# Optimization experiments

Measured on AMD Instinct MI355X. Metric: run time of the kernel, lower is better.

Reference implementation:

```python
import jax, jax.numpy as jnp
import numpy as np

# ---- model constants (from init_kwargs) ----
HIDDEN = 4096
NUM_HEADS = 32
HEAD_DIM = HIDDEN // NUM_HEADS  # 128
ROPE_THETA = 10000.0
P8 = 512
P6 = 1024
P4 = HIDDEN - P8 - P6  # 2560
BLOCK = 32  # scale-factor block size (SFB* are sized out*p//32)


def _block_quant(x, bits):
    """Symmetric per-32-element-block fake quantization along the last dim.
    Emulates the dequantized math of the packed 4/6/8-bit tiers in mixedgemm."""
    qmax = 2.0 ** (bits - 1) - 1.0
    shp = x.shape
    xb = x.reshape(shp[:-1] + (shp[-1] // BLOCK, BLOCK))
    scale = jnp.maximum(jnp.max(jnp.abs(xb), axis=-1, keepdims=True) / qmax, 1e-8)
    dq = (jnp.clip(jnp.round(xb / scale), -qmax, qmax) * scale).reshape(shp)
    return dq


def _mixed_quant(x):
    """Split reordered features into [p4 | p6 | p8] tiers and quantize each."""
    xn, xs, xo = jnp.split(x, [P4, P4 + P6], axis=-1)
    return jnp.concatenate([_block_quant(xn, 4), _block_quant(xs, 6), _block_quant(xo, 8)], axis=-1)


def _qlinear(x, W, reorder_index):
    """reorder_quantize_x + mixedgemm.matmul (dequantized reference math).
    x: [T, in], W: [out, in] (stored already in reordered column order)."""
    xq = _mixed_quant(x[..., reorder_index])
    Wq = _mixed_quant(W)
    return xq @ Wq.T


def _rotate_half(x):
    h = x.shape[-1] // 2
    return jnp.concatenate([-x[..., h:], x[..., :h]], axis=-1)


def setup_inputs() -> dict:
    key = jax.random.key(0)
    k1, k2, k3, k4, k5 = jax.random.split(key, 5)
    B, S = 2, 2048
    hidden_states = jax.random.normal(k1, (B, S, HIDDEN), dtype=jnp.float32)
    Wq = jax.random.normal(k2, (HIDDEN, HIDDEN), dtype=jnp.float32) * 0.02
    Wk = jax.random.normal(k3, (HIDDEN, HIDDEN), dtype=jnp.float32) * 0.02
    Wv = jax.random.normal(k4, (HIDDEN, HIDDEN), dtype=jnp.float32) * 0.02
    Wo = jax.random.normal(k5, (HIDDEN, HIDDEN), dtype=jnp.float32) * 0.02
    position_ids = jnp.broadcast_to(jnp.arange(S, dtype=jnp.int32)[None, :], (B, S))
    reorder_index = jnp.arange(HIDDEN, dtype=jnp.int32)  # default identity reorder
    return {"hidden_states": hidden_states, "Wq": Wq, "Wk": Wk, "Wv": Wv,
            "Wo": Wo, "position_ids": position_ids, "reorder_index": reorder_index}


def reference(hidden_states, Wq, Wk, Wv, Wo, position_ids, reorder_index):
    B, S, H = hidden_states.shape
    x2 = hidden_states.reshape(B * S, H)

    q = _qlinear(x2, Wq, reorder_index).reshape(B, S, NUM_HEADS, HEAD_DIM)
    k = _qlinear(x2, Wk, reorder_index).reshape(B, S, NUM_HEADS, HEAD_DIM)
    v = _qlinear(x2, Wv, reorder_index).reshape(B, S, NUM_HEADS, HEAD_DIM)

    # LlamaRotaryEmbedding: cos/sin [B, S, head_dim], unsqueeze_dim=2 (broadcast over heads)
    inv_freq = 1.0 / (ROPE_THETA ** (jnp.arange(0, HEAD_DIM, 2, dtype=jnp.float32) / HEAD_DIM))
    freqs = position_ids.astype(jnp.float32)[..., None] * inv_freq  # [B, S, hd/2]
    emb = jnp.concatenate([freqs, freqs], axis=-1)                  # [B, S, hd]
    cos = jnp.cos(emb)[:, :, None, :]
    sin = jnp.sin(emb)[:, :, None, :]
    q = q * cos + _rotate_half(q) * sin
    k = k * cos + _rotate_half(k) * sin

    # causal SDPA over [B, nH, S, hd]
    qh = q.transpose(0, 2, 1, 3)
    kh = k.transpose(0, 2, 1, 3)
    vh = v.transpose(0, 2, 1, 3)
    scaling = 1.0 / jnp.sqrt(jnp.float32(HEAD_DIM))
    scores = jnp.einsum('bhqd,bhkd->bhqk', qh, kh) * scaling
    causal = jnp.tril(jnp.ones((S, S), dtype=bool))
    scores = jnp.where(causal[None, None], scores, jnp.finfo(scores.dtype).min)
    probs = jax.nn.softmax(scores, axis=-1)
    attn = jnp.einsum('bhqk,bhkd->bhqd', probs, vh)  # [B, nH, S, hd]

    attn = attn.transpose(0, 2, 1, 3).reshape(B * S, H)
    out = _qlinear(attn, Wo, reorder_index).reshape(B, S, H)
    return out
```

## Files before the change

kernel.cpp:

```cpp
#include <hip/hip_runtime.h>


typedef __bf16 bf16_t;
typedef __bf16 bf16x4 __attribute__((ext_vector_type(4)));
typedef __bf16 bf16x8 __attribute__((ext_vector_type(8)));
typedef float f32x4 __attribute__((ext_vector_type(4)));

#define MFMA16(a, b, c) __builtin_amdgcn_mfma_f32_16x16x32_bf16(a, b, c, 0, 0, 0)

__device__ __forceinline__ void split_bf16(float x, bf16_t& h, bf16_t& l) {
    h = (bf16_t)x;
    l = (bf16_t)(x - (float)h);
}

typedef const __attribute__((address_space(1))) void glb_v;
typedef __attribute__((address_space(3))) void lds_v;

__device__ __forceinline__ void gl_lds16(const void* g, void* l) {
    __builtin_amdgcn_global_load_lds((glb_v*)g, (lds_v*)l, 16, 0, 0);
}
__device__ __forceinline__ void gl_lds4(const void* g, void* l) {
    __builtin_amdgcn_global_load_lds((glb_v*)g, (lds_v*)l, 4, 0, 0);
}

template<int OUT_I8>
__global__ void quant_is(const float* __restrict__ srcf,
                         const bf16_t* __restrict__ shi, const bf16_t* __restrict__ slo,
                         const int* __restrict__ rid, int src_split, int gather,
                         signed char* __restrict__ qi8, bf16_t* __restrict__ qbf,
                         float* __restrict__ qsT) {
    long idx = ((long)blockIdx.x * 256 + threadIdx.x) << 2;
    int col = (int)(idx & 4095);
    long rowoff = idx & ~4095L;
    float v[4];
    float a = 0.f;
#pragma unroll
    for (int j = 0; j < 4; ++j) {
        int g = gather ? rid[col + j] : col + j;
        float x = src_split ? ((float)shi[rowoff + g] + (float)slo[rowoff + g])
                            : srcf[rowoff + g];
        v[j] = x;
        a = fmaxf(a, fabsf(x));
    }
#pragma unroll
    for (int off = 1; off < 8; off <<= 1) a = fmaxf(a, __shfl_xor(a, off, 64));
    float qmax = (col < 2560) ? 7.0f : (col < 3584 ? 31.0f : 127.0f);
    float scale = fmaxf(a / qmax, 1e-8f);
    float inv = 1.0f / scale;
    if (OUT_I8) {
        int pk = 0;
#pragma unroll
        for (int j = 0; j < 4; ++j) {
            float q = fminf(fmaxf(rintf(v[j] * inv), -qmax), qmax);
            pk |= (int)(unsigned char)(signed char)(int)q << (8 * j);
        }
        *(int*)&qi8[idx] = pk;
    } else {
        bf16x4 pk;
#pragma unroll
        for (int j = 0; j < 4; ++j) {
            float q = fminf(fmaxf(rintf(v[j] * inv), -qmax), qmax);
            pk[j] = (bf16_t)q;
        }
        *(bf16x4*)&qbf[idx] = pk;
    }
    if ((col & 31) == 0) qsT[((long)(col >> 5) << 12) + (idx >> 12)] = scale;
}

template<int OSPL>
__global__ __launch_bounds__(256, 2) void gemm_is(
    const signed char* __restrict__ Ai, const float* __restrict__ AsT,
    const bf16_t* __restrict__ Bi, const float* __restrict__ BsT,
    bf16_t* __restrict__ OHi, bf16_t* __restrict__ OLo, float* __restrict__ Of) {
    constexpr int K = 4096, N = 4096;
    __shared__ __align__(16) bf16_t sA[2][128 * 32];
    __shared__ __align__(16) bf16_t sB[2][128 * 32];
    __shared__ __align__(16) float  sS[2][256];

    const int tid = threadIdx.x;
    const int bid = blockIdx.x;
    const int xcd = bid & 7, j = bid >> 3;
    const int bx = xcd * 4 + (j & 3), by = j >> 2;
    const int rowBase = by << 7, colBase = bx << 7;
    const int lane = tid & 63, wave = tid >> 6;
    const int wr = (wave >> 1) << 6, wc = (wave & 1) << 6;
    const int n16 = lane & 15, quad = lane >> 4;

    const int arow = tid >> 1, achk = (tid & 1) << 4;
    const long aSrc = (long)(rowBase + arow) * K + achk;
    const int aDst = arow * 64 + achk * 2;
    const int brow = tid >> 2, bchk = (tid & 3) << 3;
    const long bSrc0 = (long)(colBase + brow) * K + bchk;
    const long bSrc1 = (long)(colBase + 64 + brow) * K + bchk;
    const int bDst = tid << 4;
    const int sIsB = wave >> 1;
    const float* sPtr = (sIsB ? BsT + colBase : AsT + rowBase) + ((wave & 1) << 6) + lane;
    const int sDst = (sIsB ? 512 : 0) + ((wave & 1) << 8) + (lane << 2);

    f32x4 acc[4][4];
#pragma unroll
    for (int m = 0; m < 4; ++m)
#pragma unroll
        for (int n = 0; n < 4; ++n) acc[m][n] = (f32x4){0.f, 0.f, 0.f, 0.f};

    int4 aReg;

#define ISSUE(BUF, KB) do {                                                   \
    char* _b = (char*)sB[BUF]; char* _s = (char*)sS[BUF];                     \
    const int _k0 = (KB) << 5;                                                \
    gl_lds16(Bi + bSrc0 + _k0, _b + bDst);                                    \
    gl_lds16(Bi + bSrc1 + _k0, _b + 4096 + bDst);                             \
    gl_lds4(sPtr + ((long)(KB) << 12), _s + sDst);                            \
    aReg = *(const int4*)(Ai + aSrc + _k0);                                   \
} while (0)

#define FINISH(BUF) do {                                                      \
    asm volatile("s_waitcnt vmcnt(0)" ::: "memory");                          \
    const signed char* _pc = (const signed char*)&aReg;                       \
    bf16x8 _v0, _v1;                                                          \
    _Pragma("unroll")                                                         \
    for (int _j = 0; _j < 8; ++_j) {                                          \
        _v0[_j] = (bf16_t)(float)_pc[_j];                                     \
        _v1[_j] = (bf16_t)(float)_pc[8 + _j];                                 \
    }                                                                         \
    *(bf16x8*)((char*)sA[BUF] + aDst) = _v0;                                  \
    *(bf16x8*)((char*)sA[BUF] + aDst + 16) = _v1;                             \
    asm volatile("s_waitcnt lgkmcnt(0)" ::: "memory");                        \
    __builtin_amdgcn_s_barrier();                                             \
    asm volatile("" ::: "memory");                                            \
} while (0)

    ISSUE(0, 0);
    FINISH(0);

    for (int kb = 0; kb < 128; ++kb) {
        const int cur = kb & 1;
        if (kb < 127) ISSUE(cur ^ 1, kb + 1);

        const char* pA = (const char*)sA[cur];
        const char* pB = (const char*)sB[cur];
        const char* pS = (const char*)sS[cur];
        bf16x8 a[4], b[4];
        f32x4 asv[4];
        float bsv[4];
#pragma unroll
        for (int m = 0; m < 4; ++m) {
            a[m] = *(const bf16x8*)(pA + (wr + (m << 4) + n16) * 64 + (quad << 4));
            asv[m] = *(const f32x4*)(pS + ((wr + (m << 4) + (quad << 2)) << 2));
        }
#pragma unroll
        for (int n = 0; n < 4; ++n) {
            b[n] = *(const bf16x8*)(pB + (wc + (n << 4) + n16) * 64 + (quad << 4));
            bsv[n] = *(const float*)(pS + 512 + ((wc + (n << 4) + n16) << 2));
        }
        const f32x4 z = (f32x4){0.f, 0.f, 0.f, 0.f};
#pragma unroll
        for (int m = 0; m < 4; ++m)
#pragma unroll
            for (int n = 0; n < 4; ++n) {
                f32x4 sc = MFMA16(a[m], b[n], z);
                float bn = bsv[n];
#pragma unroll
                for (int r = 0; r < 4; ++r)
                    acc[m][n][r] = fmaf(asv[m][r] * bn, sc[r], acc[m][n][r]);
            }

        if (kb < 127) FINISH(cur ^ 1);
    }
#undef ISSUE
#undef FINISH

#pragma unroll
    for (int m = 0; m < 4; ++m)
#pragma unroll
        for (int n = 0; n < 4; ++n) {
            int row = rowBase + wr + (m << 4) + (quad << 2);
            int col = colBase + wc + (n << 4) + n16;
#pragma unroll
            for (int r = 0; r < 4; ++r) {
                if (OSPL) {
                    bf16_t h, l;
                    split_bf16(acc[m][n][r], h, l);
                    OHi[(long)(row + r) * N + col] = h;
                    OLo[(long)(row + r) * N + col] = l;
                } else {
                    Of[(long)(row + r) * N + col] = acc[m][n][r];
                }
            }
        }
}

__global__ void rope2(bf16_t* __restrict__ qh, bf16_t* __restrict__ ql,
                      bf16_t* __restrict__ kh, bf16_t* __restrict__ kl,
                      const int* __restrict__ pos) {
    int t = blockIdx.x;
    int tid = threadIdx.x;
    __shared__ float cs[64], sn[64];
    if (tid < 64) {
        float invf = (float)pow(10000.0, -(double)tid / 64.0);
        float ang = (float)pos[t] * invf;
        cs[tid] = (float)cos((double)ang);
        sn[tid] = (float)sin((double)ang);
    }
    __syncthreads();
#pragma unroll
    for (int i = 0; i < 8; ++i) {
        int l = i * 256 + tid;
        int hh = l >> 6, d = l & 63;
        long base = (long)t * 4096 + hh * 128 + d;
        float c = cs[d], s = sn[d];
        float a0 = (float)qh[base] + (float)ql[base];
        float a1 = (float)qh[base + 64] + (float)ql[base + 64];
        float r0 = a0 * c - a1 * s, r1 = a1 * c + a0 * s;
        bf16_t x, y;
        split_bf16(r0, x, y); qh[base] = x;      ql[base] = y;
        split_bf16(r1, x, y); qh[base + 64] = x; ql[base + 64] = y;
        float b0 = (float)kh[base] + (float)kl[base];
        float b1 = (float)kh[base + 64] + (float)kl[base + 64];
        r0 = b0 * c - b1 * s; r1 = b1 * c + b0 * s;
        split_bf16(r0, x, y); kh[base] = x;      kl[base] = y;
        split_bf16(r1, x, y); kh[base + 64] = x; kl[base + 64] = y;
    }
}

__global__ void transpose_vt(const ushort* __restrict__ vh, const ushort* __restrict__ vl,
                             ushort* __restrict__ th, ushort* __restrict__ tl) {
    __shared__ ushort t0[64][68];
    __shared__ ushort t1[64][68];
    int ct = blockIdx.x, tt = blockIdx.y, tid = threadIdx.x;
#pragma unroll
    for (int i = 0; i < 16; ++i) {
        int l = i * 256 + tid, r = l >> 6, c = l & 63;
        long idx = (long)(tt * 64 + r) * 4096 + ct * 64 + c;
        t0[r][c] = vh[idx];
        t1[r][c] = vl[idx];
    }
    __syncthreads();
#pragma unroll
    for (int i = 0; i < 16; ++i) {
        int l = i * 256 + tid, dr = l >> 6, sc = l & 63;
        int colg = ct * 64 + dr, hh = colg >> 7, dl = colg & 127;
        int tok = tt * 64 + sc, b = tok >> 11, s = tok & 2047;
        long o = (long)((b * 32 + hh) * 128 + dl) * 2048 + s;
        th[o] = t0[sc][dr];
        tl[o] = t1[sc][dr];
    }
}

__global__ __launch_bounds__(256, 2) void flash_attn3(
    const bf16_t* __restrict__ qhp, const bf16_t* __restrict__ qlp,
    const bf16_t* __restrict__ khp, const bf16_t* __restrict__ klp,
    const bf16_t* __restrict__ vth, const bf16_t* __restrict__ vtl,
    bf16_t* __restrict__ ohi, bf16_t* __restrict__ olo) {
    __shared__ __align__(16) char smem[75776];

    const int bid = blockIdx.x;
    const int xcd = bid & 7, ixd = bid >> 3;
    const int bh = (xcd << 3) + (ixd >> 4);
    const int qt = 15 - (ixd & 15);
    const int b = bh >> 5, h = bh & 31;
    const int tid = threadIdx.x;
    const int wave = tid >> 6, lane = tid & 63;
    const int n16 = lane & 15, quad = lane >> 4;
    const long tokB = (long)b * 2048;
    const int q0 = qt * 128 + wave * 32;
    const float scale = 0.08838834764831845f;

    bf16_t (*pH)[40] = (bf16_t (*)[40])(smem + 65536 + wave * 2560);
    bf16_t (*pL)[40] = (bf16_t (*)[40])(smem + 65536 + wave * 2560 + 1280);

    bf16x8 qhF[2][4], qlF[2][4];
#pragma unroll
    for (int m = 0; m < 2; ++m) {
        long qoff = (tokB + q0 + m * 16 + n16) * 4096 + h * 128 + quad * 8;
#pragma unroll
        for (int f = 0; f < 4; ++f) {
            qhF[m][f] = *(const bf16x8*)&qhp[qoff + f * 32];
            qlF[m][f] = *(const bf16x8*)&qlp[qoff + f * 32];
        }
    }

    const int kr0 = wave * 8 + quad;
    const int kc0 = ((((lane & 15) << 4) ^ (quad << 4)) >> 1);
    const int kc1 = ((((lane & 15) << 4) ^ ((4 + quad) << 4)) >> 1);
    const int kd0 = kr0 * 256 + ((lane & 15) << 4);
    const int vr0 = wave * 32 + (lane >> 2);
    const int vc0 = ((((lane & 3) << 4) ^ (((lane >> 2) & 3) << 4)) >> 1);
    const int vd0 = vr0 * 64 + ((lane & 3) << 4);
    const long vrow_g = (long)(bh * 128 + vr0) * 2048;

#define STAGE(BUF, KB) do {                                                   \
    char* _bb = smem + ((BUF) << 15);                                         \
    const long _kt = tokB + (long)(KB) * 32;                                  \
    const long _g0 = (_kt + kr0) * 4096 + h * 128;                            \
    gl_lds16(khp + _g0 + kc0,           _bb + kd0);                           \
    gl_lds16(klp + _g0 + kc0,           _bb + 8192 + kd0);                    \
    gl_lds16(khp + _g0 + 4 * 4096 + kc1, _bb + 1024 + kd0);                   \
    gl_lds16(klp + _g0 + 4 * 4096 + kc1, _bb + 8192 + 1024 + kd0);            \
    const long _v0 = vrow_g + (KB) * 32 + vc0;                                \
    gl_lds16(vth + _v0,                 _bb + 16384 + vd0);                   \
    gl_lds16(vtl + _v0,                 _bb + 24576 + vd0);                   \
    gl_lds16(vth + _v0 + 16 * 2048,     _bb + 16384 + 1024 + vd0);            \
    gl_lds16(vtl + _v0 + 16 * 2048,     _bb + 24576 + 1024 + vd0);            \
} while (0)

    f32x4 o[2][8];
#pragma unroll
    for (int m = 0; m < 2; ++m)
#pragma unroll
        for (int dc = 0; dc < 8; ++dc) o[m][dc] = (f32x4){0.f, 0.f, 0.f, 0.f};
    float m_i[2][4], l_i[2][4];
#pragma unroll
    for (int m = 0; m < 2; ++m)
#pragma unroll
        for (int r = 0; r < 4; ++r) { m_i[m][r] = -1e30f; l_i[m][r] = 0.f; }

    const int nkb = 4 * qt + 4;
    const int lastkb = 4 * qt + wave;

    STAGE(0, 0);
    asm volatile("s_waitcnt vmcnt(0)" ::: "memory");
    __builtin_amdgcn_s_barrier();
    asm volatile("" ::: "memory");

    for (int kb = 0; kb < nkb; ++kb) {
        if (kb + 1 < nkb) STAGE((kb + 1) & 1, kb + 1);

        if (kb <= lastkb) {
            const char* bK = smem + ((kb & 1) << 15);
            const char* bV = bK + 16384;

            f32x4 s[2][2];
            const int rswz = (n16 & 7) << 4;
#pragma unroll
            for (int nt = 0; nt < 2; ++nt) {
                const int krow = nt * 16 + n16;
                bf16x8 kh[4], kl[4];
#pragma unroll
                for (int f = 0; f < 4; ++f) {
                    const int cb = ((f << 6) | (quad << 4)) ^ rswz;
                    kh[f] = *(const bf16x8*)(bK + krow * 256 + cb);
                    kl[f] = *(const bf16x8*)(bK + 8192 + krow * 256 + cb);
                }
#pragma unroll
                for (int m = 0; m < 2; ++m) {
                    f32x4 sc = (f32x4){0.f, 0.f, 0.f, 0.f};
#pragma unroll
                    for (int f = 0; f < 4; ++f) {
                        sc = MFMA16(qhF[m][f], kh[f], sc);
                        sc = MFMA16(qhF[m][f], kl[f], sc);
                        sc = MFMA16(qlF[m][f], kh[f], sc);
                    }
                    s[m][nt] = sc;
                }
            }

            if (kb == lastkb) {
                const int key0 = kb * 32 + n16;
#pragma unroll
                for (int m = 0; m < 2; ++m)
#pragma unroll
                    for (int nt = 0; nt < 2; ++nt)
#pragma unroll
                        for (int r = 0; r < 4; ++r) {
                            int qrow = q0 + m * 16 + quad * 4 + r;
                            s[m][nt][r] = (key0 + nt * 16 <= qrow) ? s[m][nt][r] * scale
                                                                   : -1e30f;
                        }
            } else {
#pragma unroll
                for (int m = 0; m < 2; ++m)
#pragma unroll
                    for (int nt = 0; nt < 2; ++nt)
#pragma unroll
                        for (int r = 0; r < 4; ++r) s[m][nt][r] *= scale;
            }

            float alpha[2][4];
#pragma unroll
            for (int m = 0; m < 2; ++m)
#pragma unroll
                for (int r = 0; r < 4; ++r) {
                    float mx = fmaxf(s[m][0][r], s[m][1][r]);
#pragma unroll
                    for (int off = 1; off < 16; off <<= 1) mx = fmaxf(mx, __shfl_xor(mx, off, 64));
                    float mnew = fmaxf(m_i[m][r], mx);
                    alpha[m][r] = expf(m_i[m][r] - mnew);
                    m_i[m][r] = mnew;
                    float p0 = expf(s[m][0][r] - mnew);
                    float p1 = expf(s[m][1][r] - mnew);
                    s[m][0][r] = p0;
                    s[m][1][r] = p1;
                    float sum = p0 + p1;
#pragma unroll
                    for (int off = 1; off < 16; off <<= 1) sum += __shfl_xor(sum, off, 64);
                    l_i[m][r] = l_i[m][r] * alpha[m][r] + sum;
                }

            bf16x8 ph2[2], pl2[2];
#pragma unroll
            for (int m = 0; m < 2; ++m) {
#pragma unroll
                for (int nt = 0; nt < 2; ++nt)
#pragma unroll
                    for (int r = 0; r < 4; ++r) {
                        bf16_t hh2, ll2;
                        split_bf16(s[m][nt][r], hh2, ll2);
                        pH[quad * 4 + r][nt * 16 + n16] = hh2;
                        pL[quad * 4 + r][nt * 16 + n16] = ll2;
                    }
                ph2[m] = *(const bf16x8*)&pH[n16][quad * 8];
                pl2[m] = *(const bf16x8*)&pL[n16][quad * 8];
            }

#pragma unroll
            for (int dc = 0; dc < 8; ++dc) {
                const int vrow = dc * 16 + n16;
                const int vcb = ((quad ^ (n16 & 3)) << 4);
                bf16x8 vh = *(const bf16x8*)(bV + vrow * 64 + vcb);
                bf16x8 vl = *(const bf16x8*)(bV + 8192 + vrow * 64 + vcb);
#pragma unroll
                for (int m = 0; m < 2; ++m) {
#pragma unroll
                    for (int r = 0; r < 4; ++r) o[m][dc][r] *= alpha[m][r];
                    o[m][dc] = MFMA16(ph2[m], vh, o[m][dc]);
                    o[m][dc] = MFMA16(ph2[m], vl, o[m][dc]);
                    o[m][dc] = MFMA16(pl2[m], vh, o[m][dc]);
                }
            }
        }

        asm volatile("s_waitcnt vmcnt(0)" ::: "memory");
        __builtin_amdgcn_s_barrier();
        asm volatile("" ::: "memory");
    }
#undef STAGE

#pragma unroll
    for (int m = 0; m < 2; ++m)
#pragma unroll
        for (int r = 0; r < 4; ++r) {
            float invl = 1.0f / l_i[m][r];
            long row = tokB + q0 + m * 16 + quad * 4 + r;
#pragma unroll
            for (int dc = 0; dc < 8; ++dc) {
                bf16_t hh2, ll2;
                split_bf16(o[m][dc][r] * invl, hh2, ll2);
                ohi[row * 4096 + h * 128 + dc * 16 + n16] = hh2;
                olo[row * 4096 + h * 128 + dc * 16 + n16] = ll2;
            }
        }
}

extern "C" void kernel_launch(void* const* d_in, const int* in_sizes, int n_in,
                              void* d_out, int out_size, void* d_ws, size_t ws_size,
                              hipStream_t stream) {
    const float* x  = (const float*)d_in[0];
    const float* Wq = (const float*)d_in[1];
    const float* Wk = (const float*)d_in[2];
    const float* Wv = (const float*)d_in[3];
    const float* Wo = (const float*)d_in[4];
    const int* pos  = (const int*)d_in[5];
    const int* rid  = (const int*)d_in[6];

    const size_t MB = 1024ull * 1024ull;
    char* ws = (char*)d_ws;
    bf16_t* QH = (bf16_t*)(ws);
    bf16_t* QL = (bf16_t*)(ws + 32 * MB);
    bf16_t* KH = (bf16_t*)(ws + 64 * MB);
    bf16_t* KL = (bf16_t*)(ws + 96 * MB);
    signed char* Xi = (signed char*)(ws + 128 * MB);
    float*  XsT = (float*)(ws + 144 * MB);
    float*  WsT = (float*)(ws + 146 * MB);
    bf16_t* Wi  = (bf16_t*)(ws + 160 * MB);
    bf16_t* VTh = (bf16_t*)(ws + 128 * MB);
    bf16_t* VTl = (bf16_t*)(ws + 160 * MB);
    signed char* Xi2 = (signed char*)(ws + 64 * MB);
    float*  Xs2T = (float*)(ws + 96 * MB);
    bf16_t* Wo_i = (bf16_t*)(ws + 128 * MB);
    float*  WoST = (float*)(ws + 160 * MB);
    bf16_t* OUh = (bf16_t*)d_out;
    bf16_t* OUl = (bf16_t*)((char*)d_out + 32 * MB);

    const int QG = 16384;

    quant_is<1><<<QG, 256, 0, stream>>>(x, nullptr, nullptr, rid, 0, 1, Xi, nullptr, XsT);

    quant_is<0><<<QG, 256, 0, stream>>>(Wq, nullptr, nullptr, rid, 0, 0, nullptr, Wi, WsT);
    gemm_is<1><<<1024, 256, 0, stream>>>(Xi, XsT, Wi, WsT, QH, QL, nullptr);
    quant_is<0><<<QG, 256, 0, stream>>>(Wk, nullptr, nullptr, rid, 0, 0, nullptr, Wi, WsT);
    gemm_is<1><<<1024, 256, 0, stream>>>(Xi, XsT, Wi, WsT, KH, KL, nullptr);
    quant_is<0><<<QG, 256, 0, stream>>>(Wv, nullptr, nullptr, rid, 0, 0, nullptr, Wi, WsT);
    gemm_is<1><<<1024, 256, 0, stream>>>(Xi, XsT, Wi, WsT, OUh, OUl, nullptr);

    rope2<<<4096, 256, 0, stream>>>(QH, QL, KH, KL, pos);

    transpose_vt<<<dim3(64, 64), 256, 0, stream>>>((const ushort*)OUh, (const ushort*)OUl,
                                                   (ushort*)VTh, (ushort*)VTl);

    flash_attn3<<<1024, 256, 0, stream>>>(QH, QL, KH, KL, VTh, VTl, OUh, OUl);

    quant_is<1><<<QG, 256, 0, stream>>>(nullptr, OUh, OUl, rid, 1, 1, Xi2, nullptr, Xs2T);
    quant_is<0><<<QG, 256, 0, stream>>>(Wo, nullptr, nullptr, rid, 0, 0, nullptr, Wo_i, WoST);
    gemm_is<0><<<1024, 256, 0, stream>>>(Xi2, Xs2T, Wo_i, WoST, nullptr, nullptr, (float*)d_out);

    (void)in_sizes; (void)n_in; (void)out_size; (void)ws_size;
}
```

Measured before the change: 2.381 ms.

## Triple-buffer and swizzle GEMM, vectorize quant/rope/transpose, add MFMA priority hints

New measurement: 2.186 ms. -8.2%, faster.

```diff
diff --git a/kernel.cpp b/kernel.cpp
--- a/kernel.cpp
+++ b/kernel.cpp
@@ -23,10 +23,10 @@
     __builtin_amdgcn_global_load_lds((glb_v*)g, (lds_v*)l, 4, 0, 0);
 }
 
-template<int OUT_I8>
+template<int OUT_I8, int SPLIT, int GATHER>
 __global__ void quant_is(const float* __restrict__ srcf,
                          const bf16_t* __restrict__ shi, const bf16_t* __restrict__ slo,
-                         const int* __restrict__ rid, int src_split, int gather,
+                         const int* __restrict__ rid,
                          signed char* __restrict__ qi8, bf16_t* __restrict__ qbf,
                          float* __restrict__ qsT) {
     long idx = ((long)blockIdx.x * 256 + threadIdx.x) << 2;
@@ -34,13 +34,20 @@
     long rowoff = idx & ~4095L;
     float v[4];
     float a = 0.f;
-#pragma unroll
-    for (int j = 0; j < 4; ++j) {
-        int g = gather ? rid[col + j] : col + j;
-        float x = src_split ? ((float)shi[rowoff + g] + (float)slo[rowoff + g])
+    if (!GATHER && !SPLIT) {
+        float4 f = *(const float4*)&srcf[idx];
+        v[0] = f.x; v[1] = f.y; v[2] = f.z; v[3] = f.w;
+#pragma unroll
+        for (int j = 0; j < 4; ++j) a = fmaxf(a, fabsf(v[j]));
+    } else {
+#pragma unroll
+        for (int j = 0; j < 4; ++j) {
+            int g = GATHER ? rid[col + j] : col + j;
+            float x = SPLIT ? ((float)shi[rowoff + g] + (float)slo[rowoff + g])
                             : srcf[rowoff + g];
-        v[j] = x;
-        a = fmaxf(a, fabsf(x));
+            v[j] = x;
+            a = fmaxf(a, fabsf(x));
+        }
     }
 #pragma unroll
     for (int off = 1; off < 8; off <<= 1) a = fmaxf(a, __shfl_xor(a, off, 64));
@@ -73,25 +80,29 @@
     const bf16_t* __restrict__ Bi, const float* __restrict__ BsT,
     bf16_t* __restrict__ OHi, bf16_t* __restrict__ OLo, float* __restrict__ Of) {
     constexpr int K = 4096, N = 4096;
-    __shared__ __align__(16) bf16_t sA[2][128 * 32];
-    __shared__ __align__(16) bf16_t sB[2][128 * 32];
-    __shared__ __align__(16) float  sS[2][256];
+    __shared__ __align__(16) bf16_t sA[3][128 * 32];
+    __shared__ __align__(16) bf16_t sB[3][128 * 32];
+    __shared__ __align__(16) float  sS[3][256];
 
     const int tid = threadIdx.x;
     const int bid = blockIdx.x;
-    const int xcd = bid & 7, j = bid >> 3;
-    const int bx = xcd * 4 + (j & 3), by = j >> 2;
+    const int xcd = bid & 7, jj = bid >> 3;
+    const int bx = xcd * 4 + (jj & 3), by = jj >> 2;
     const int rowBase = by << 7, colBase = bx << 7;
     const int lane = tid & 63, wave = tid >> 6;
     const int wr = (wave >> 1) << 6, wc = (wave & 1) << 6;
     const int n16 = lane & 15, quad = lane >> 4;
 
-    const int arow = tid >> 1, achk = (tid & 1) << 4;
-    const long aSrc = (long)(rowBase + arow) * K + achk;
-    const int aDst = arow * 64 + achk * 2;
-    const int brow = tid >> 2, bchk = (tid & 3) << 3;
-    const long bSrc0 = (long)(colBase + brow) * K + bchk;
-    const long bSrc1 = (long)(colBase + 64 + brow) * K + bchk;
+    const int arow = tid >> 1, acb = (tid & 1) << 4;
+    const long aSrc = (long)(rowBase + arow) * K + acb;
+    const int aswz = (arow & 3) << 4;
+    const int ac0 = (acb >> 3) << 4;
+    const int aDst0 = arow * 64 + (ac0 ^ aswz);
+    const int aDst1 = arow * 64 + ((ac0 + 16) ^ aswz);
+    const int brow = tid >> 2;
+    const int bcs = (((tid & 3) ^ (brow & 3)) << 3);
+    const long bSrc0 = (long)(colBase + brow) * K + bcs;
+    const long bSrc1 = (long)(colBase + 64 + brow) * K + bcs;
     const int bDst = tid << 4;
     const int sIsB = wave >> 1;
     const float* sPtr = (sIsB ? BsT + colBase : AsT + rowBase) + ((wave & 1) << 6) + lane;
@@ -103,72 +114,104 @@
 #pragma unroll
         for (int n = 0; n < 4; ++n) acc[m][n] = (f32x4){0.f, 0.f, 0.f, 0.f};
 
-    int4 aReg;
-
-#define ISSUE(BUF, KB) do {                                                   \
-    char* _b = (char*)sB[BUF]; char* _s = (char*)sS[BUF];                     \
-    const int _k0 = (KB) << 5;                                                \
+    int4 aRegA, aRegB;
+
+#define ISSUE(BUFI, KB, AR) do {                                              \
+    char* _b = (char*)sB[BUFI];                                               \
+    char* _s = (char*)sS[BUFI];                                               \
+    const long _k0 = (long)(KB) << 5;                                         \
     gl_lds16(Bi + bSrc0 + _k0, _b + bDst);                                    \
     gl_lds16(Bi + bSrc1 + _k0, _b + 4096 + bDst);                             \
     gl_lds4(sPtr + ((long)(KB) << 12), _s + sDst);                            \
-    aReg = *(const int4*)(Ai + aSrc + _k0);                                   \
+    AR = *(const int4*)(Ai + aSrc + _k0);                                     \
 } while (0)
 
-#define FINISH(BUF) do {                                                      \
-    asm volatile("s_waitcnt vmcnt(0)" ::: "memory");                          \
-    const signed char* _pc = (const signed char*)&aReg;                       \
+#define CVTW(BUFI, AR) do {                                                   \
+    const signed char* _pc = (const signed char*)&AR;                         \
     bf16x8 _v0, _v1;                                                          \
     _Pragma("unroll")                                                         \
-    for (int _j = 0; _j < 8; ++_j) {                                          \
-        _v0[_j] = (bf16_t)(float)_pc[_j];                                     \
-        _v1[_j] = (bf16_t)(float)_pc[8 + _j];                                 \
+    for (int _j2 = 0; _j2 < 8; ++_j2) {                                       \
+        _v0[_j2] = (bf16_t)(float)_pc[_j2];                                   \
+        _v1[_j2] = (bf16_t)(float)_pc[8 + _j2];                               \
     }                                                                         \
-    *(bf16x8*)((char*)sA[BUF] + aDst) = _v0;                                  \
-    *(bf16x8*)((char*)sA[BUF] + aDst + 16) = _v1;                             \
-    asm volatile("s_waitcnt lgkmcnt(0)" ::: "memory");                        \
-    __builtin_amdgcn_s_barrier();                                             \
-    asm volatile("" ::: "memory");                                            \
+    *(bf16x8*)((char*)sA[BUFI] + aDst0) = _v0;                                \
+    *(bf16x8*)((char*)sA[BUFI] + aDst1) = _v1;                                \
 } while (0)
 
-    ISSUE(0, 0);
-    FINISH(0);
-
-    for (int kb = 0; kb < 128; ++kb) {
-        const int cur = kb & 1;
-        if (kb < 127) ISSUE(cur ^ 1, kb + 1);
-
-        const char* pA = (const char*)sA[cur];
-        const char* pB = (const char*)sB[cur];
-        const char* pS = (const char*)sS[cur];
-        bf16x8 a[4], b[4];
-        f32x4 asv[4];
-        float bsv[4];
-#pragma unroll
-        for (int m = 0; m < 4; ++m) {
-            a[m] = *(const bf16x8*)(pA + (wr + (m << 4) + n16) * 64 + (quad << 4));
-            asv[m] = *(const f32x4*)(pS + ((wr + (m << 4) + (quad << 2)) << 2));
-        }
-#pragma unroll
-        for (int n = 0; n < 4; ++n) {
-            b[n] = *(const bf16x8*)(pB + (wc + (n << 4) + n16) * 64 + (quad << 4));
-            bsv[n] = *(const float*)(pS + 512 + ((wc + (n << 4) + n16) << 2));
-        }
-        const f32x4 z = (f32x4){0.f, 0.f, 0.f, 0.f};
-#pragma unroll
-        for (int m = 0; m < 4; ++m)
-#pragma unroll
-            for (int n = 0; n < 4; ++n) {
-                f32x4 sc = MFMA16(a[m], b[n], z);
-                float bn = bsv[n];
-#pragma unroll
-                for (int r = 0; r < 4; ++r)
-                    acc[m][n][r] = fmaf(asv[m][r] * bn, sc[r], acc[m][n][r]);
-            }
-
-        if (kb < 127) FINISH(cur ^ 1);
+#define WAITV(NN) asm volatile("s_waitcnt vmcnt(" #NN ")" ::: "memory")
+#define BARR() do { asm volatile("s_waitcnt lgkmcnt(0)" ::: "memory");        \
+    __builtin_amdgcn_s_barrier(); asm volatile("" ::: "memory"); } while (0)
+
+#define COMPUTE(BUFI) do {                                                    \
+    const char* _pA = (const char*)sA[BUFI];                                  \
+    const char* _pB = (const char*)sB[BUFI];                                  \
+    const float* _pS = sS[BUFI];                                              \
+    const int _rsw = (n16 & 3) << 4;                                          \
+    bf16x8 _a[4], _bv[4];                                                     \
+    f32x4 _as[4];                                                             \
+    float _bs[4];                                                             \
+    _Pragma("unroll")                                                         \
+    for (int _m = 0; _m < 4; ++_m) {                                          \
+        _a[_m] = *(const bf16x8*)(_pA + (wr + (_m << 4) + n16) * 64           \
+                                  + ((quad << 4) ^ _rsw));                    \
+        _as[_m] = *(const f32x4*)(_pS + wr + (_m << 4) + (quad << 2));        \
+    }                                                                         \
+    _Pragma("unroll")                                                         \
+    for (int _n = 0; _n < 4; ++_n) {                                          \
+        _bv[_n] = *(const bf16x8*)(_pB + (wc + (_n << 4) + n16) * 64          \
+                                   + ((quad << 4) ^ _rsw));                   \
+        _bs[_n] = _pS[128 + wc + (_n << 4) + n16];                            \
+    }                                                                         \
+    const f32x4 _z = (f32x4){0.f, 0.f, 0.f, 0.f};                             \
+    _Pragma("unroll")                                                         \
+    for (int _m = 0; _m < 4; ++_m)                                            \
+        _Pragma("unroll")                                                     \
+        for (int _n = 0; _n < 4; ++_n) {                                      \
+            f32x4 _sc = MFMA16(_a[_m], _bv[_n], _z);                          \
+            float _bn = _bs[_n];                                              \
+            _Pragma("unroll")                                                 \
+            for (int _r = 0; _r < 4; ++_r)                                    \
+                acc[_m][_n][_r] = fmaf(_as[_m][_r] * _bn, _sc[_r],            \
+                                       acc[_m][_n][_r]);                      \
+        }                                                                     \
+} while (0)
+
+    ISSUE(0, 0, aRegA);
+    ISSUE(1, 1, aRegB);
+    WAITV(4);
+    CVTW(0, aRegA);
+    BARR();
+
+    int bc = 0;
+    for (int kb = 0; kb < 128; kb += 2) {
+        int b1 = bc + 1; if (b1 >= 3) b1 -= 3;
+        int b2 = bc + 2; if (b2 >= 3) b2 -= 3;
+        if (kb + 2 < 128) {
+            ISSUE(b2, kb + 2, aRegA);
+            COMPUTE(bc);
+            WAITV(4);
+        } else {
+            COMPUTE(bc);
+            WAITV(0);
+        }
+        CVTW(b1, aRegB);
+        BARR();
+        if (kb + 3 < 128) {
+            ISSUE(bc, kb + 3, aRegB);
+            COMPUTE(b1);
+            WAITV(4);
+            CVTW(b2, aRegA);
+            BARR();
+        } else {
+            COMPUTE(b1);
+        }
+        bc = b2;
     }
 #undef ISSUE
-#undef FINISH
+#undef CVTW
+#undef WAITV
+#undef BARR
+#undef COMPUTE
 
 #pragma unroll
     for (int m = 0; m < 4; ++m)
@@ -203,47 +246,66 @@
         sn[tid] = (float)sin((double)ang);
     }
     __syncthreads();
-#pragma unroll
-    for (int i = 0; i < 8; ++i) {
-        int l = i * 256 + tid;
-        int hh = l >> 6, d = l & 63;
-        long base = (long)t * 4096 + hh * 128 + d;
-        float c = cs[d], s = sn[d];
-        float a0 = (float)qh[base] + (float)ql[base];
-        float a1 = (float)qh[base + 64] + (float)ql[base + 64];
+    const int hh = tid >> 3, d0 = (tid & 7) << 3;
+    const long base = (long)t * 4096 + hh * 128 + d0;
+    bf16x8 q0 = *(const bf16x8*)&qh[base],      q1 = *(const bf16x8*)&qh[base + 64];
+    bf16x8 ql0 = *(const bf16x8*)&ql[base],     ql1 = *(const bf16x8*)&ql[base + 64];
+    bf16x8 k0 = *(const bf16x8*)&kh[base],      k1 = *(const bf16x8*)&kh[base + 64];
+    bf16x8 kl0 = *(const bf16x8*)&kl[base],     kl1 = *(const bf16x8*)&kl[base + 64];
+    bf16x8 oqh0, oqh1, oql0, oql1, okh0, okh1, okl0, okl1;
+#pragma unroll
+    for (int j = 0; j < 8; ++j) {
+        float c = cs[d0 + j], s = sn[d0 + j];
+        float a0 = (float)q0[j] + (float)ql0[j];
+        float a1 = (float)q1[j] + (float)ql1[j];
         float r0 = a0 * c - a1 * s, r1 = a1 * c + a0 * s;
         bf16_t x, y;
-        split_bf16(r0, x, y); qh[base] = x;      ql[base] = y;
-        split_bf16(r1, x, y); qh[base + 64] = x; ql[base + 64] = y;
-        float b0 = (float)kh[base] + (float)kl[base];
-        float b1 = (float)kh[base + 64] + (float)kl[base + 64];
+        split_bf16(r0, x, y); oqh0[j] = x; oql0[j] = y;
+        split_bf16(r1, x, y); oqh1[j] = x; oql1[j] = y;
+        float b0 = (float)k0[j] + (float)kl0[j];
+        float b1 = (float)k1[j] + (float)kl1[j];
         r0 = b0 * c - b1 * s; r1 = b1 * c + b0 * s;
-        split_bf16(r0, x, y); kh[base] = x;      kl[base] = y;
-        split_bf16(r1, x, y); kh[base + 64] = x; kl[base + 64] = y;
-    }
+        split_bf16(r0, x, y); okh0[j] = x; okl0[j] = y;
+        split_bf16(r1, x, y); okh1[j] = x; okl1[j] = y;
+    }
+    *(bf16x8*)&qh[base] = oqh0;      *(bf16x8*)&qh[base + 64] = oqh1;
+    *(bf16x8*)&ql[base] = oql0;      *(bf16x8*)&ql[base + 64] = oql1;
+    *(bf16x8*)&kh[base] = okh0;      *(bf16x8*)&kh[base + 64] = okh1;
+    *(bf16x8*)&kl[base] = okl0;      *(bf16x8*)&kl[base + 64] = okl1;
 }
 
 __global__ void transpose_vt(const ushort* __restrict__ vh, const ushort* __restrict__ vl,
                              ushort* __restrict__ th, ushort* __restrict__ tl) {
-    __shared__ ushort t0[64][68];
-    __shared__ ushort t1[64][68];
-    int ct = blockIdx.x, tt = blockIdx.y, tid = threadIdx.x;
-#pragma unroll
-    for (int i = 0; i < 16; ++i) {
-        int l = i * 256 + tid, r = l >> 6, c = l & 63;
-        long idx = (long)(tt * 64 + r) * 4096 + ct * 64 + c;
-        t0[r][c] = vh[idx];
-        t1[r][c] = vl[idx];
+    __shared__ __align__(16) ushort t0[64 * 72];
+    __shared__ __align__(16) ushort t1[64 * 72];
+    const int ct = blockIdx.x, tt = blockIdx.y, tid = threadIdx.x;
+#pragma unroll
+    for (int i = 0; i < 2; ++i) {
+        int cid = i * 256 + tid;
+        int r = cid >> 3, c8 = cid & 7;
+        long g = (long)(tt * 64 + r) * 4096 + ct * 64 + c8 * 8;
+        int d = r * 144 + ((c8 << 4) ^ (((r >> 3) & 7) << 4));
+        *(uint4*)((char*)t0 + d) = *(const uint4*)&vh[g];
+        *(uint4*)((char*)t1 + d) = *(const uint4*)&vl[g];
     }
     __syncthreads();
 #pragma unroll
-    for (int i = 0; i < 16; ++i) {
-        int l = i * 256 + tid, dr = l >> 6, sc = l & 63;
+    for (int i = 0; i < 2; ++i) {
+        int cid = i * 256 + tid;
+        int dr = cid >> 3, s8 = cid & 7;
         int colg = ct * 64 + dr, hh = colg >> 7, dl = colg & 127;
-        int tok = tt * 64 + sc, b = tok >> 11, s = tok & 2047;
+        int tok0 = tt * 64 + s8 * 8, b = tok0 >> 11, s = tok0 & 2047;
         long o = (long)((b * 32 + hh) * 128 + dl) * 2048 + s;
-        th[o] = t0[sc][dr];
-        tl[o] = t1[sc][dr];
+        ushort u0[8], u1[8];
+#pragma unroll
+        for (int jk = 0; jk < 8; ++jk) {
+            int r = s8 * 8 + jk;
+            int byt = r * 144 + (((dr >> 3) << 4) ^ (((r >> 3) & 7) << 4)) + (dr & 7) * 2;
+            u0[jk] = *(const ushort*)((const char*)t0 + byt);
+            u1[jk] = *(const ushort*)((const char*)t1 + byt);
+        }
+        *(uint4*)&th[o] = *(const uint4*)u0;
+        *(uint4*)&tl[o] = *(const uint4*)u1;
     }
 }
 
@@ -332,6 +394,7 @@
 
             f32x4 s[2][2];
             const int rswz = (n16 & 7) << 4;
+            __builtin_amdgcn_s_setprio(1);
 #pragma unroll
             for (int nt = 0; nt < 2; ++nt) {
                 const int krow = nt * 16 + n16;
@@ -354,6 +417,7 @@
                     s[m][nt] = sc;
                 }
             }
+            __builtin_amdgcn_s_setprio(0);
 
             if (kb == lastkb) {
                 const int key0 = kb * 32 + n16;
@@ -413,6 +477,7 @@
                 pl2[m] = *(const bf16x8*)&pL[n16][quad * 8];
             }
 
+            __builtin_amdgcn_s_setprio(1);
 #pragma unroll
             for (int dc = 0; dc < 8; ++dc) {
                 const int vrow = dc * 16 + n16;
@@ -428,6 +493,7 @@
                     o[m][dc] = MFMA16(pl2[m], vh, o[m][dc]);
                 }
             }
+            __builtin_amdgcn_s_setprio(0);
         }
 
         asm volatile("s_waitcnt vmcnt(0)" ::: "memory");
@@ -484,13 +550,13 @@
 
     const int QG = 16384;
 
-    quant_is<1><<<QG, 256, 0, stream>>>(x, nullptr, nullptr, rid, 0, 1, Xi, nullptr, XsT);
-
-    quant_is<0><<<QG, 256, 0, stream>>>(Wq, nullptr, nullptr, rid, 0, 0, nullptr, Wi, WsT);
+    quant_is<1, 0, 1><<<QG, 256, 0, stream>>>(x, nullptr, nullptr, rid, Xi, nullptr, XsT);
+
+    quant_is<0, 0, 0><<<QG, 256, 0, stream>>>(Wq, nullptr, nullptr, rid, nullptr, Wi, WsT);
     gemm_is<1><<<1024, 256, 0, stream>>>(Xi, XsT, Wi, WsT, QH, QL, nullptr);
-    quant_is<0><<<QG, 256, 0, stream>>>(Wk, nullptr, nullptr, rid, 0, 0, nullptr, Wi, WsT);
+    quant_is<0, 0, 0><<<QG, 256, 0, stream>>>(Wk, nullptr, nullptr, rid, nullptr, Wi, WsT);
     gemm_is<1><<<1024, 256, 0, stream>>>(Xi, XsT, Wi, WsT, KH, KL, nullptr);
-    quant_is<0><<<QG, 256, 0, stream>>>(Wv, nullptr, nullptr, rid, 0, 0, nullptr, Wi, WsT);
+    quant_is<0, 0, 0><<<QG, 256, 0, stream>>>(Wv, nullptr, nullptr, rid, nullptr, Wi, WsT);
     gemm_is<1><<<1024, 256, 0, stream>>>(Xi, XsT, Wi, WsT, OUh, OUl, nullptr);
 
     rope2<<<4096, 256, 0, stream>>>(QH, QL, KH, KL, pos);
@@ -500,8 +566,8 @@
 
     flash_attn3<<<1024, 256, 0, stream>>>(QH, QL, KH, KL, VTh, VTl, OUh, OUl);
 
-    quant_is<1><<<QG, 256, 0, stream>>>(nullptr, OUh, OUl, rid, 1, 1, Xi2, nullptr, Xs2T);
-    quant_is<0><<<QG, 256, 0, stream>>>(Wo, nullptr, nullptr, rid, 0, 0, nullptr, Wo_i, WoST);
+    quant_is<1, 1, 1><<<QG, 256, 0, stream>>>(nullptr, OUh, OUl, rid, Xi2, nullptr, Xs2T);
+    quant_is<0, 0, 0><<<QG, 256, 0, stream>>>(Wo, nullptr, nullptr, rid, nullptr, Wo_i, WoST);
     gemm_is<0><<<1024, 256, 0, stream>>>(Xi2, Xs2T, Wo_i, WoST, nullptr, nullptr, (float*)d_out);
 
     (void)in_sizes; (void)n_in; (void)out_size; (void)ws_size;
```
